# Performance work log

Hardware: AMD Instinct MI355X
Metric: run time of the kernel (lower is better)

The kernel has to match this reference:

```python
import jax, jax.numpy as jnp
import numpy as np

BN_EPS = 1e-5


def gcn_conv(x, src, dst, ew, W, b, n_nodes):
    # PyG GCNConv: xW, then D^-1/2 (A+I) D^-1/2 aggregation (self-loop weight 1), then +bias
    xw = x @ W                                                  # [N, out]
    deg = jax.ops.segment_sum(ew, dst, num_segments=n_nodes) + 1.0  # includes self-loop
    dinv = jax.lax.rsqrt(deg)                                   # [N]
    norm = dinv[src] * ew * dinv[dst]                           # [E]
    agg = jax.ops.segment_sum(xw[src] * norm[:, None], dst, num_segments=n_nodes)
    agg = agg + xw * (1.0 / deg)[:, None]                       # self-loop term: dinv_i*1*dinv_i = 1/deg_i
    return agg + b


def batch_norm(h, gamma, beta):
    # training-mode BatchNorm1d: batch statistics (biased variance)
    mean = jnp.mean(h, axis=0)
    var = jnp.mean((h - mean) ** 2, axis=0)
    return (h - mean) * jax.lax.rsqrt(var + BN_EPS) * gamma + beta


def setup_inputs() -> dict:
    key = jax.random.key(0)
    ks = jax.random.split(key, 12)
    N, E, F_IN, H1, H2 = 100000, 1600000, 128, 64, 32
    x = jax.random.normal(ks[0], (N, F_IN), dtype=jnp.float32)
    edge_index = jax.random.randint(ks[1], (2, E), 0, N, dtype=jnp.int64)
    edge_weight = jax.random.uniform(ks[2], (E,), dtype=jnp.float32)
    W1 = jax.random.normal(ks[3], (F_IN, H1), dtype=jnp.float32) / np.sqrt(F_IN)
    b1 = jnp.zeros((H1,), dtype=jnp.float32)
    W2 = jax.random.normal(ks[4], (H1, H2), dtype=jnp.float32) / np.sqrt(H1)
    b2 = jnp.zeros((H2,), dtype=jnp.float32)
    g1 = jnp.ones((H1,), dtype=jnp.float32)
    be1 = jnp.zeros((H1,), dtype=jnp.float32)
    g2 = jnp.ones((H2,), dtype=jnp.float32)
    be2 = jnp.zeros((H2,), dtype=jnp.float32)
    Wl = jax.random.normal(ks[5], (H2, 1), dtype=jnp.float32) / np.sqrt(H2)
    bl = jnp.zeros((1,), dtype=jnp.float32)
    return {"x": x, "edge_index": edge_index, "edge_weight": edge_weight,
            "W1": W1, "b1": b1, "g1": g1, "be1": be1,
            "W2": W2, "b2": b2, "g2": g2, "be2": be2,
            "Wl": Wl, "bl": bl}


def reference(x, edge_index, edge_weight, W1, b1, g1, be1, W2, b2, g2, be2, Wl, bl):
    n_nodes = x.shape[0]
    src, dst = edge_index[0], edge_index[1]
    h = gcn_conv(x, src, dst, edge_weight, W1, b1, n_nodes)
    h = jax.nn.relu(batch_norm(h, g1, be1))          # dropout = identity (eval)
    h = gcn_conv(h, src, dst, edge_weight, W2, b2, n_nodes)
    h = jax.nn.relu(batch_norm(h, g2, be2))
    return (h @ Wl + bl).squeeze(-1)                 # [N]
```

## Files before the change

kernel.cpp:

```cpp
#include <hip/hip_runtime.h>
#include <hip/hip_bf16.h>

#define FIN 128
#define C1 64
#define C2 32
#define BN_EPS 1e-5f
#define CAP 28
#define OVFCAP 65536
#define R1 16
#define R2 16

typedef __hip_bfloat16 bf16;

__global__ __launch_bounds__(256) void k_degfill(const int* __restrict__ ei, const float* __restrict__ ew,
                                                 float* __restrict__ deg, int* __restrict__ pcnt,
                                                 int* __restrict__ pad, int* __restrict__ ovf,
                                                 int* __restrict__ ovfn, int E) {
  int e = blockIdx.x * 256 + threadIdx.x;
  if (e < E) {
    int dst = ei[E + e];
    atomicAdd(&deg[dst], ew[e]);
    int pos = atomicAdd(&pcnt[dst], 1);
    if (pos < CAP) {
      pad[(size_t)dst * CAP + pos] = e;
    } else {
      int oi = atomicAdd(ovfn, 1);
      if (oi < OVFCAP) ovf[oi] = e;
    }
  }
}

__global__ __launch_bounds__(256) void k_dinv(float* __restrict__ deg, int N) {
  int i = blockIdx.x * 256 + threadIdx.x;
  if (i < N) deg[i] = rsqrtf(deg[i] + 1.0f);
}

__global__ __launch_bounds__(256) void k_gemm1(const float* __restrict__ x, const float* __restrict__ W1,
                                               bf16* __restrict__ xw1, int N) {
  const int lane = threadIdx.x & 63;
  const int w = threadIdx.x >> 6;
  float wr[32];
#pragma unroll
  for (int kk = 0; kk < 32; ++kk) wr[kk] = W1[(32 * w + kk) * C1 + lane];
  __shared__ float xs[R1][FIN];
  __shared__ float part[R1][4][C1];
  for (int base = blockIdx.x * R1; base < N; base += gridDim.x * R1) {
    int nrows = min(R1, N - base);
    __syncthreads();
    for (int t = threadIdx.x; t < nrows * FIN; t += 256) {
      int r = t >> 7, k = t & 127;
      xs[r][k] = x[(size_t)(base + r) * FIN + k];
    }
    __syncthreads();
#pragma unroll 4
    for (int r = 0; r < R1; ++r) {
      if (r >= nrows) break;
      const float* xrow = &xs[r][32 * w];
      float acc = 0.f;
#pragma unroll
      for (int kk = 0; kk < 32; kk += 4) {
        float4 xv = *(const float4*)&xrow[kk];
        acc = fmaf(xv.x, wr[kk], acc);
        acc = fmaf(xv.y, wr[kk + 1], acc);
        acc = fmaf(xv.z, wr[kk + 2], acc);
        acc = fmaf(xv.w, wr[kk + 3], acc);
      }
      part[r][w][lane] = acc;
    }
    __syncthreads();
    for (int t = threadIdx.x; t < nrows * C1; t += 256) {
      int r = t >> 6, c = t & 63;
      float v = (part[r][0][c] + part[r][1][c]) + (part[r][2][c] + part[r][3][c]);
      xw1[(size_t)(base + r) * C1 + c] = __float2bfloat16(v);
    }
  }
}

__global__ __launch_bounds__(256) void k_agg1(const int* __restrict__ pcnt, const int* __restrict__ pad,
                                              const int* __restrict__ ei, const float* __restrict__ ew,
                                              const float* __restrict__ dinv, const bf16* __restrict__ xw,
                                              const float* __restrict__ b, float* __restrict__ h, int N, int E) {
  const int lane = threadIdx.x & 63;
  const int wid = (blockIdx.x * 256 + threadIdx.x) >> 6;
  const int nw = (gridDim.x * 256) >> 6;
  for (int dst = wid; dst < N; dst += nw) {
    float dv = dinv[dst];
    float acc = fmaf(__bfloat162float(xw[(size_t)dst * C1 + lane]), dv * dv, b[lane]);
    int c = pcnt[dst];
    c = c < CAP ? c : CAP;
    int sv = 0;
    float nv = 0.f;
    if (lane < c) {
      int eid = pad[(size_t)dst * CAP + lane];
      sv = ei[eid];
      nv = dinv[sv] * ew[eid] * dv;
    }
    for (int k = 0; k < c; ++k) {
      int s = __shfl(sv, k);
      float nm = __shfl(nv, k);
      acc = fmaf(__bfloat162float(xw[(size_t)s * C1 + lane]), nm, acc);
    }
    h[(size_t)dst * C1 + lane] = acc;
  }
}

__global__ __launch_bounds__(256) void k_ovf1(const int* __restrict__ ovf, const int* __restrict__ ovfn,
                                              const int* __restrict__ ei, const float* __restrict__ ew,
                                              const float* __restrict__ dinv, const bf16* __restrict__ xw,
                                              float* __restrict__ h, int E) {
  const int lane = threadIdx.x & 63;
  const int wid = (blockIdx.x * 256 + threadIdx.x) >> 6;
  const int nw = (gridDim.x * 256) >> 6;
  int n = ovfn[0];
  n = n < OVFCAP ? n : OVFCAP;
  for (int i = wid; i < n; i += nw) {
    int eid = ovf[i];
    int src = ei[eid];
    int dst = ei[E + eid];
    float nrm = dinv[src] * ew[eid] * dinv[dst];
    atomicAdd(&h[(size_t)dst * C1 + lane], __bfloat162float(xw[(size_t)src * C1 + lane]) * nrm);
  }
}

__global__ __launch_bounds__(256) void k_agg2(const int* __restrict__ pcnt, const int* __restrict__ pad,
                                              const int* __restrict__ ei, const float* __restrict__ ew,
                                              const float* __restrict__ dinv, const float* __restrict__ xw,
                                              const float* __restrict__ b, float* __restrict__ h, int N, int E) {
  const int lane = threadIdx.x & 63;
  const int j = lane & 31, sub = lane >> 5;
  const int wid = (blockIdx.x * 256 + threadIdx.x) >> 6;
  const int nw = (gridDim.x * 256) >> 6;
  for (int dst = wid; dst < N; dst += nw) {
    float dv = dinv[dst];
    float acc = (sub == 0) ? fmaf(xw[(size_t)dst * C2 + j], dv * dv, b[j]) : 0.f;
    int c = pcnt[dst];
    c = c < CAP ? c : CAP;
    int sv = 0;
    float nv = 0.f;
    if (lane < c) {
      int eid = pad[(size_t)dst * CAP + lane];
      sv = ei[eid];
      nv = dinv[sv] * ew[eid] * dv;
    }
    for (int k = sub; k < c; k += 2) {
      int s = __shfl(sv, k);
      float nm = __shfl(nv, k);
      acc = fmaf(xw[(size_t)s * C2 + j], nm, acc);
    }
    acc += __shfl_xor(acc, 32);
    if (sub == 0) h[(size_t)dst * C2 + j] = acc;
  }
}

__global__ __launch_bounds__(256) void k_ovf2(const int* __restrict__ ovf, const int* __restrict__ ovfn,
                                              const int* __restrict__ ei, const float* __restrict__ ew,
                                              const float* __restrict__ dinv, const float* __restrict__ xw,
                                              float* __restrict__ h, int E) {
  const int lane = threadIdx.x & 63;
  const int wid = (blockIdx.x * 256 + threadIdx.x) >> 6;
  const int nw = (gridDim.x * 256) >> 6;
  int n = ovfn[0];
  n = n < OVFCAP ? n : OVFCAP;
  for (int i = wid; i < n; i += nw) {
    int eid = ovf[i];
    int src = ei[eid];
    int dst = ei[E + eid];
    float nrm = dinv[src] * ew[eid] * dinv[dst];
    if (lane < C2) atomicAdd(&h[(size_t)dst * C2 + lane], xw[(size_t)src * C2 + lane] * nrm);
  }
}

template <int C>
__global__ __launch_bounds__(256) void k_bnstats(const float* __restrict__ h, float* __restrict__ stat, int N) {
  const int rpb = 256 / C;
  const int j = threadIdx.x % C;
  const int rloc = threadIdx.x / C;
  float s = 0.f, sq = 0.f;
  for (int r = blockIdx.x * rpb + rloc; r < N; r += gridDim.x * rpb) {
    float v = h[(size_t)r * C + j];
    s += v;
    sq = fmaf(v, v, sq);
  }
  __shared__ float ls[256], lq[256];
  ls[threadIdx.x] = s;
  lq[threadIdx.x] = sq;
  __syncthreads();
  if (threadIdx.x < C) {
    float ts = 0.f, tq = 0.f;
#pragma unroll
    for (int k = 0; k < rpb; ++k) {
      ts += ls[k * C + j];
      tq += lq[k * C + j];
    }
    atomicAdd(&stat[j], ts);
    atomicAdd(&stat[C + j], tq);
  }
}

template <int C>
__global__ void k_bnfinal(const float* __restrict__ stat, const float* __restrict__ g,
                          const float* __restrict__ be, float* __restrict__ ss, int N) {
  int j = threadIdx.x;
  if (j < C) {
    float inv_n = 1.0f / (float)N;
    float mean = stat[j] * inv_n;
    float var = stat[C + j] * inv_n - mean * mean;
    float sc = g[j] * rsqrtf(var + BN_EPS);
    ss[j] = sc;
    ss[C + j] = be[j] - mean * sc;
  }
}

template <int C>
__global__ __launch_bounds__(256) void k_bnapply(float* __restrict__ h, const float* __restrict__ ss, int N) {
  int total = N * C;
  for (int t = blockIdx.x * 256 + threadIdx.x; t < total; t += gridDim.x * 256) {
    int j = t % C;
    float v = fmaf(h[t], ss[j], ss[C + j]);
    h[t] = v > 0.f ? v : 0.f;
  }
}

__global__ __launch_bounds__(256) void k_gemm2(const float* __restrict__ h1, const float* __restrict__ W2,
                                               float* __restrict__ xw2, int N) {
  const int lane = threadIdx.x & 63;
  const int w = threadIdx.x >> 6;
  const int c = lane & 31, hh = lane >> 5;
  const int slice = w * 2 + hh;
  float wr[8];
#pragma unroll
  for (int kk = 0; kk < 8; ++kk) wr[kk] = W2[(8 * slice + kk) * C2 + c];
  __shared__ float xs[R2][C1];
  __shared__ float part[R2][8][C2];
  for (int base = blockIdx.x * R2; base < N; base += gridDim.x * R2) {
    int nrows = min(R2, N - base);
    __syncthreads();
    for (int t = threadIdx.x; t < nrows * C1; t += 256) {
      int r = t >> 6, k = t & 63;
      xs[r][k] = h1[(size_t)(base + r) * C1 + k];
    }
    __syncthreads();
#pragma unroll 4
    for (int r = 0; r < R2; ++r) {
      if (r >= nrows) break;
      const float* xrow = &xs[r][8 * slice];
      float4 a = *(const float4*)&xrow[0];
      float4 bb = *(const float4*)&xrow[4];
      float acc = a.x * wr[0];
      acc = fmaf(a.y, wr[1], acc);
      acc = fmaf(a.z, wr[2], acc);
      acc = fmaf(a.w, wr[3], acc);
      acc = fmaf(bb.x, wr[4], acc);
      acc = fmaf(bb.y, wr[5], acc);
      acc = fmaf(bb.z, wr[6], acc);
      acc = fmaf(bb.w, wr[7], acc);
      part[r][slice][c] = acc;
    }
    __syncthreads();
    for (int t = threadIdx.x; t < nrows * C2; t += 256) {
      int r = t >> 5, cc = t & 31;
      float v = 0.f;
#pragma unroll
      for (int s = 0; s < 8; ++s) v += part[r][s][cc];
      xw2[(size_t)(base + r) * C2 + cc] = v;
    }
  }
}

__global__ __launch_bounds__(256) void k_head(const float* __restrict__ h2, const float* __restrict__ Wl,
                                              const float* __restrict__ bl, float* __restrict__ out, int N) {
  const int lane = threadIdx.x & 63;
  const int j = lane & 31, sub = lane >> 5;
  const int wid = (blockIdx.x * 256 + threadIdx.x) >> 6;
  const int nw = (gridDim.x * 256) >> 6;
  float wv = Wl[j];
  float blv = bl[0];
  for (int r0 = wid * 2; r0 < N; r0 += nw * 2) {
    int row = r0 + sub;
    float v = (row < N) ? h2[(size_t)row * C2 + j] * wv : 0.f;
    v += __shfl_down(v, 16, 32);
    v += __shfl_down(v, 8, 32);
    v += __shfl_down(v, 4, 32);
    v += __shfl_down(v, 2, 32);
    v += __shfl_down(v, 1, 32);
    if (j == 0 && row < N) out[row] = v + blv;
  }
}

extern "C" void kernel_launch(void* const* d_in, const int* in_sizes, int n_in,
                              void* d_out, int out_size, void* d_ws, size_t ws_size,
                              hipStream_t stream) {
  const float* x = (const float*)d_in[0];
  const int* ei = (const int*)d_in[1];
  const float* ew = (const float*)d_in[2];
  const float* W1 = (const float*)d_in[3];
  const float* b1 = (const float*)d_in[4];
  const float* g1 = (const float*)d_in[5];
  const float* be1 = (const float*)d_in[6];
  const float* W2 = (const float*)d_in[7];
  const float* b2 = (const float*)d_in[8];
  const float* g2 = (const float*)d_in[9];
  const float* be2 = (const float*)d_in[10];
  const float* Wl = (const float*)d_in[11];
  const float* bl = (const float*)d_in[12];
  float* out = (float*)d_out;

  const int N = in_sizes[0] / FIN;
  const int E = in_sizes[2];

  float* Wf = (float*)d_ws;
  float* dinv = Wf;
  int* pcnt = (int*)(Wf + N);
  int* ovfn = (int*)(Wf + 2 * (size_t)N);
  float* stat1 = Wf + 2 * (size_t)N + 8;
  float* ss1 = stat1 + 128;
  float* stat2 = ss1 + 128;
  float* ss2 = stat2 + 64;
  int* ovf = (int*)(Wf + 2 * (size_t)N + 512);
  int* pad = ovf + OVFCAP;
  bf16* xw1 = (bf16*)(pad + (size_t)N * CAP);
  float* bufB = (float*)(xw1 + (size_t)N * C1);
  float* h1 = bufB;
  float* xw2 = (float*)xw1;
  float* h2 = bufB;

  hipMemsetAsync(Wf, 0, ((size_t)2 * N + 512) * sizeof(float), stream);

  k_degfill<<<(E + 255) / 256, 256, 0, stream>>>(ei, ew, dinv, pcnt, pad, ovf, ovfn, E);
  k_dinv<<<(N + 255) / 256, 256, 0, stream>>>(dinv, N);

  k_gemm1<<<2048, 256, 0, stream>>>(x, W1, xw1, N);
  k_agg1<<<4096, 256, 0, stream>>>(pcnt, pad, ei, ew, dinv, xw1, b1, h1, N, E);
  k_ovf1<<<256, 256, 0, stream>>>(ovf, ovfn, ei, ew, dinv, xw1, h1, E);
  k_bnstats<C1><<<1024, 256, 0, stream>>>(h1, stat1, N);
  k_bnfinal<C1><<<1, C1, 0, stream>>>(stat1, g1, be1, ss1, N);
  k_bnapply<C1><<<4096, 256, 0, stream>>>(h1, ss1, N);

  k_gemm2<<<2048, 256, 0, stream>>>(h1, W2, xw2, N);
  k_agg2<<<2048, 256, 0, stream>>>(pcnt, pad, ei, ew, dinv, xw2, b2, h2, N, E);
  k_ovf2<<<256, 256, 0, stream>>>(ovf, ovfn, ei, ew, dinv, xw2, h2, E);
  k_bnstats<C2><<<1024, 256, 0, stream>>>(h2, stat2, N);
  k_bnfinal<C2><<<1, C2, 0, stream>>>(stat2, g2, be2, ss2, N);
  k_bnapply<C2><<<2048, 256, 0, stream>>>(h2, ss2, N);

  k_head<<<1024, 256, 0, stream>>>(h2, Wl, bl, out, N);
}
```

Before: 663.1 us.

## Fuse BN apply into consumers and compute degree from padded adjacency

```diff
diff --git a/kernel.cpp b/kernel.cpp
--- a/kernel.cpp
+++ b/kernel.cpp
@@ -12,14 +12,12 @@
 
 typedef __hip_bfloat16 bf16;
 
-__global__ __launch_bounds__(256) void k_degfill(const int* __restrict__ ei, const float* __restrict__ ew,
-                                                 float* __restrict__ deg, int* __restrict__ pcnt,
+__global__ __launch_bounds__(256) void k_fillpad(const int* __restrict__ ei, int* __restrict__ pcnt,
                                                  int* __restrict__ pad, int* __restrict__ ovf,
                                                  int* __restrict__ ovfn, int E) {
   int e = blockIdx.x * 256 + threadIdx.x;
   if (e < E) {
     int dst = ei[E + e];
-    atomicAdd(&deg[dst], ew[e]);
     int pos = atomicAdd(&pcnt[dst], 1);
     if (pos < CAP) {
       pad[(size_t)dst * CAP + pos] = e;
@@ -30,9 +28,28 @@
   }
 }
 
-__global__ __launch_bounds__(256) void k_dinv(float* __restrict__ deg, int N) {
+__global__ __launch_bounds__(256) void k_ovfdeg(const int* __restrict__ ovf, const int* __restrict__ ovfn,
+                                                const int* __restrict__ ei, const float* __restrict__ ew,
+                                                float* __restrict__ deg, int E) {
+  int n = ovfn[0];
+  n = n < OVFCAP ? n : OVFCAP;
+  for (int i = blockIdx.x * 256 + threadIdx.x; i < n; i += gridDim.x * 256) {
+    int eid = ovf[i];
+    atomicAdd(&deg[ei[E + eid]], ew[eid]);
+  }
+}
+
+__global__ __launch_bounds__(256) void k_degdinv(const int* __restrict__ pcnt, const int* __restrict__ pad,
+                                                 const float* __restrict__ ew, float* __restrict__ deg, int N) {
   int i = blockIdx.x * 256 + threadIdx.x;
-  if (i < N) deg[i] = rsqrtf(deg[i] + 1.0f);
+  if (i < N) {
+    int c = pcnt[i];
+    c = c < CAP ? c : CAP;
+    float s = deg[i] + 1.0f;
+    const int* row = pad + (size_t)i * CAP;
+    for (int k = 0; k < c; ++k) s += ew[row[k]];
+    deg[i] = rsqrtf(s);
+  }
 }
 
 __global__ __launch_bounds__(256) void k_gemm1(const float* __restrict__ x, const float* __restrict__ W1,
@@ -211,18 +228,8 @@
   }
 }
 
-template <int C>
-__global__ __launch_bounds__(256) void k_bnapply(float* __restrict__ h, const float* __restrict__ ss, int N) {
-  int total = N * C;
-  for (int t = blockIdx.x * 256 + threadIdx.x; t < total; t += gridDim.x * 256) {
-    int j = t % C;
-    float v = fmaf(h[t], ss[j], ss[C + j]);
-    h[t] = v > 0.f ? v : 0.f;
-  }
-}
-
-__global__ __launch_bounds__(256) void k_gemm2(const float* __restrict__ h1, const float* __restrict__ W2,
-                                               float* __restrict__ xw2, int N) {
+__global__ __launch_bounds__(256) void k_gemm2(const float* __restrict__ h1, const float* __restrict__ ss,
+                                               const float* __restrict__ W2, float* __restrict__ xw2, int N) {
   const int lane = threadIdx.x & 63;
   const int w = threadIdx.x >> 6;
   const int c = lane & 31, hh = lane >> 5;
@@ -230,6 +237,8 @@
   float wr[8];
 #pragma unroll
   for (int kk = 0; kk < 8; ++kk) wr[kk] = W2[(8 * slice + kk) * C2 + c];
+  __shared__ float sss[2 * C1];
+  if (threadIdx.x < 2 * C1) sss[threadIdx.x] = ss[threadIdx.x];
   __shared__ float xs[R2][C1];
   __shared__ float part[R2][8][C2];
   for (int base = blockIdx.x * R2; base < N; base += gridDim.x * R2) {
@@ -237,7 +246,8 @@
     __syncthreads();
     for (int t = threadIdx.x; t < nrows * C1; t += 256) {
       int r = t >> 6, k = t & 63;
-      xs[r][k] = h1[(size_t)(base + r) * C1 + k];
+      float v = fmaf(h1[(size_t)(base + r) * C1 + k], sss[k], sss[C1 + k]);
+      xs[r][k] = v > 0.f ? v : 0.f;
     }
     __syncthreads();
 #pragma unroll 4
@@ -267,17 +277,24 @@
   }
 }
 
-__global__ __launch_bounds__(256) void k_head(const float* __restrict__ h2, const float* __restrict__ Wl,
-                                              const float* __restrict__ bl, float* __restrict__ out, int N) {
+__global__ __launch_bounds__(256) void k_head(const float* __restrict__ h2, const float* __restrict__ ss,
+                                              const float* __restrict__ Wl, const float* __restrict__ bl,
+                                              float* __restrict__ out, int N) {
   const int lane = threadIdx.x & 63;
   const int j = lane & 31, sub = lane >> 5;
   const int wid = (blockIdx.x * 256 + threadIdx.x) >> 6;
   const int nw = (gridDim.x * 256) >> 6;
-  float wv = Wl[j];
-  float blv = bl[0];
+  const float sc = ss[j], sh = ss[C2 + j];
+  const float wv = Wl[j];
+  const float blv = bl[0];
   for (int r0 = wid * 2; r0 < N; r0 += nw * 2) {
     int row = r0 + sub;
-    float v = (row < N) ? h2[(size_t)row * C2 + j] * wv : 0.f;
+    float v = 0.f;
+    if (row < N) {
+      float hh = fmaf(h2[(size_t)row * C2 + j], sc, sh);
+      hh = hh > 0.f ? hh : 0.f;
+      v = hh * wv;
+    }
     v += __shfl_down(v, 16, 32);
     v += __shfl_down(v, 8, 32);
     v += __shfl_down(v, 4, 32);
@@ -326,22 +343,21 @@
 
   hipMemsetAsync(Wf, 0, ((size_t)2 * N + 512) * sizeof(float), stream);
 
-  k_degfill<<<(E + 255) / 256, 256, 0, stream>>>(ei, ew, dinv, pcnt, pad, ovf, ovfn, E);
-  k_dinv<<<(N + 255) / 256, 256, 0, stream>>>(dinv, N);
+  k_fillpad<<<(E + 255) / 256, 256, 0, stream>>>(ei, pcnt, pad, ovf, ovfn, E);
+  k_ovfdeg<<<16, 256, 0, stream>>>(ovf, ovfn, ei, ew, dinv, E);
+  k_degdinv<<<(N + 255) / 256, 256, 0, stream>>>(pcnt, pad, ew, dinv, N);
 
   k_gemm1<<<2048, 256, 0, stream>>>(x, W1, xw1, N);
   k_agg1<<<4096, 256, 0, stream>>>(pcnt, pad, ei, ew, dinv, xw1, b1, h1, N, E);
   k_ovf1<<<256, 256, 0, stream>>>(ovf, ovfn, ei, ew, dinv, xw1, h1, E);
   k_bnstats<C1><<<1024, 256, 0, stream>>>(h1, stat1, N);
   k_bnfinal<C1><<<1, C1, 0, stream>>>(stat1, g1, be1, ss1, N);
-  k_bnapply<C1><<<4096, 256, 0, stream>>>(h1, ss1, N);
-
-  k_gemm2<<<2048, 256, 0, stream>>>(h1, W2, xw2, N);
+
+  k_gemm2<<<2048, 256, 0, stream>>>(h1, ss1, W2, xw2, N);
   k_agg2<<<2048, 256, 0, stream>>>(pcnt, pad, ei, ew, dinv, xw2, b2, h2, N, E);
   k_ovf2<<<256, 256, 0, stream>>>(ovf, ovfn, ei, ew, dinv, xw2, h2, E);
   k_bnstats<C2><<<1024, 256, 0, stream>>>(h2, stat2, N);
   k_bnfinal<C2><<<1, C2, 0, stream>>>(stat2, g2, be2, ss2, N);
-  k_bnapply<C2><<<2048, 256, 0, stream>>>(h2, ss2, N);
-
-  k_head<<<1024, 256, 0, stream>>>(h2, Wl, bl, out, N);
-}
+
+  k_head<<<1024, 256, 0, stream>>>(h2, ss2, Wl, bl, out, N);
+}
```

Result: no change. 650.7 us (-1.9%).
